# Performance work log

Measured on AMD Instinct MI355X. Metric: run time of the kernel, lower is better.

## Reference

```python
import jax, jax.numpy as jnp
import numpy as np

B, S, E, H = 4, 2048, 1024, 16
HD = E // H


def setup_inputs() -> dict:
    key = jax.random.key(0)
    ks = jax.random.split(key, 7)
    scale = 1.0 / np.sqrt(E)
    return {
        "query": jax.random.normal(ks[0], (B, S, E), dtype=jnp.float32),
        "key": jax.random.normal(ks[1], (B, S, E), dtype=jnp.float32),
        "value": jax.random.normal(ks[2], (B, S, E), dtype=jnp.float32),
        "Wqkv": jax.random.normal(ks[3], (3 * E, E), dtype=jnp.float32) * scale,
        "bqkv": jnp.zeros((3 * E,), dtype=jnp.float32),
        "Wout": jax.random.normal(ks[4], (E, E), dtype=jnp.float32) * scale,
        "bout": jnp.zeros((E,), dtype=jnp.float32),
    }


def reference(query, key, value, Wqkv, bqkv, Wout, bout):
    # key/value are ignored by the original module (QKV all from query).
    b, s, e = query.shape
    qkv = query @ Wqkv.T + bqkv                       # [B,S,3E]
    qkv = qkv.reshape(b, s, 3, H, HD)
    q = jnp.transpose(qkv[:, :, 0], (0, 2, 1, 3))     # [B,H,S,HD]
    k = jnp.transpose(qkv[:, :, 1], (0, 2, 1, 3))
    v = jnp.transpose(qkv[:, :, 2], (0, 2, 1, 3))
    # NOTE: original scales by embed_dim**0.5, not head_dim**0.5
    scores = jnp.einsum("bhqd,bhkd->bhqk", q, k) / jnp.sqrt(jnp.float32(e))
    attn = jax.nn.softmax(scores, axis=-1)            # dropout = identity (eval)
    out = jnp.einsum("bhqk,bhkd->bhqd", attn, v)      # [B,H,S,HD]
    out = jnp.transpose(out, (0, 2, 1, 3)).reshape(b, s, e)
    return out @ Wout.T + bout
```

## Files before the change

kernel.cpp:

```cpp
#include <hip/hip_runtime.h>
#include <stdint.h>


typedef __bf16 bf16;
typedef __bf16 bf16x8 __attribute__((ext_vector_type(8)));
typedef __bf16 bf16x4 __attribute__((ext_vector_type(4)));
typedef float  f32x4  __attribute__((ext_vector_type(4)));
typedef float  f32x16 __attribute__((ext_vector_type(16)));
typedef unsigned u32x2 __attribute__((ext_vector_type(2)));
typedef unsigned u32x4 __attribute__((ext_vector_type(4)));

#define MFMA16(a, b, c) __builtin_amdgcn_mfma_f32_16x16x32_bf16((a), (b), (c), 0, 0, 0)
#define MFMA32(a, b, c) __builtin_amdgcn_mfma_f32_32x32x16_bf16((a), (b), (c), 0, 0, 0)

__device__ __forceinline__ void gload16(const void* g, void* l) {
  __builtin_amdgcn_global_load_lds(
      (const __attribute__((address_space(1))) void*)g,
      (__attribute__((address_space(3))) void*)l, 16, 0, 0);
}

__device__ __forceinline__ uint32_t lds_off(const void* p) {
  return (uint32_t)(uintptr_t)(__attribute__((address_space(3))) const void*)p;
}

template <int IMM>
__device__ __forceinline__ bf16x4 tr16o(uint32_t off) {
  bf16x4 d;
  asm volatile("ds_read_b64_tr_b16 %0, %1 offset:%2" : "=&v"(d) : "v"(off), "i"(IMM));
  return d;
}

__device__ __forceinline__ bf16x8 vpack(bf16x4 lo, bf16x4 hi) {
  const u32x2 a = __builtin_bit_cast(u32x2, lo);
  const u32x2 b = __builtin_bit_cast(u32x2, hi);
  u32x4 t;
  t[0] = a[0]; t[1] = a[1]; t[2] = b[0]; t[3] = b[1];
  return __builtin_bit_cast(bf16x8, t);
}

__global__ __launch_bounds__(256) void cvt_all(const float* __restrict__ a,
                                               const float* __restrict__ b,
                                               const float* __restrict__ c,
                                               bf16* __restrict__ out,
                                               int na4, int nb4, int nc4) {
  const int i = blockIdx.x * 256 + threadIdx.x;
  const float4* src;
  int j = i;
  if (i < na4) {
    src = (const float4*)a;
  } else if (i < na4 + nb4) {
    src = (const float4*)b; j = i - na4;
  } else if (i < na4 + nb4 + nc4) {
    src = (const float4*)c; j = i - na4 - nb4;
  } else {
    return;
  }
  const float4 v = src[j];
  bf16x4 o;
  o[0] = (bf16)v.x; o[1] = (bf16)v.y; o[2] = (bf16)v.z; o[3] = (bf16)v.w;
  ((bf16x4*)out)[i] = o;
}

template <typename OutT>
__global__ __launch_bounds__(256, 2) void gemm_bt(const bf16* __restrict__ A,
                                                  const bf16* __restrict__ Bt,
                                                  const float* __restrict__ bias,
                                                  OutT* __restrict__ C,
                                                  int M, int N, int K,
                                                  int sc_lo, int sc_hi, float scv) {
  __shared__ bf16 As[2][128 * 32];
  __shared__ bf16 Bs[2][128 * 32];
  const int tid = threadIdx.x;
  const int lane = tid & 63, wid = tid >> 6;
  const int l15 = lane & 15, lg = lane >> 4;
  const int wr = wid >> 1, wc = wid & 1;
  const int row0 = blockIdx.y * 128, col0 = blockIdx.x * 128;
  const float cscale = (col0 >= sc_lo && col0 < sc_hi) ? scv : 1.0f;

  const char* asrc[2]; const char* bsrc[2];
  int ado[2];
#pragma unroll
  for (int j = 0; j < 2; ++j) {
    const int c = j * 256 + tid;
    const int r = c >> 2, cb = (c & 3) << 4;
    asrc[j] = (const char*)(A + (size_t)(row0 + r) * K) + cb;
    bsrc[j] = (const char*)(Bt + (size_t)(col0 + r) * K) + cb;
    ado[j] = c * 16;
  }

  f32x4 acc[4][4];
#pragma unroll
  for (int m = 0; m < 4; ++m)
#pragma unroll
    for (int n = 0; n < 4; ++n) acc[m][n] = (f32x4){0.f, 0.f, 0.f, 0.f};

  const int nIt = K >> 5;

  gload16(asrc[0], (char*)&As[0][0] + ado[0]);
  gload16(asrc[1], (char*)&As[0][0] + ado[1]);
  gload16(bsrc[0], (char*)&Bs[0][0] + ado[0]);
  gload16(bsrc[1], (char*)&Bs[0][0] + ado[1]);

  for (int it = 0; it < nIt; ++it) {
    const int cur = it & 1;
    if (it < nIt - 1) {
      const size_t off = (size_t)(it + 1) * 64;
      gload16(asrc[0] + off, (char*)&As[cur ^ 1][0] + ado[0]);
      gload16(asrc[1] + off, (char*)&As[cur ^ 1][0] + ado[1]);
      gload16(bsrc[0] + off, (char*)&Bs[cur ^ 1][0] + ado[0]);
      gload16(bsrc[1] + off, (char*)&Bs[cur ^ 1][0] + ado[1]);
      __builtin_amdgcn_sched_barrier(0);
      asm volatile("s_waitcnt vmcnt(4)" ::: "memory");
    } else {
      __builtin_amdgcn_sched_barrier(0);
      asm volatile("s_waitcnt vmcnt(0)" ::: "memory");
    }
    __builtin_amdgcn_s_barrier();
    __builtin_amdgcn_sched_barrier(0);

    const bf16* as = &As[cur][0];
    const bf16* bs = &Bs[cur][0];
    bf16x8 af[4], bfr[4];
#pragma unroll
    for (int m = 0; m < 4; ++m)
      af[m] = *(const bf16x8*)(as + ((wr * 64 + m * 16 + l15) << 5) + lg * 8);
#pragma unroll
    for (int n = 0; n < 4; ++n)
      bfr[n] = *(const bf16x8*)(bs + ((wc * 64 + n * 16 + l15) << 5) + lg * 8);
    __builtin_amdgcn_s_setprio(1);
#pragma unroll
    for (int m = 0; m < 4; ++m)
#pragma unroll
      for (int n = 0; n < 4; ++n) acc[m][n] = MFMA16(af[m], bfr[n], acc[m][n]);
    __builtin_amdgcn_s_setprio(0);
    __builtin_amdgcn_sched_barrier(0);
    __builtin_amdgcn_s_barrier();
  }

#pragma unroll
  for (int m = 0; m < 4; ++m) {
    const int grow0 = row0 + wr * 64 + m * 16 + lg * 4;
#pragma unroll
    for (int n = 0; n < 4; ++n) {
      const int gcol = col0 + wc * 64 + n * 16 + l15;
      const float bv = bias[gcol];
#pragma unroll
      for (int i = 0; i < 4; ++i)
        C[(size_t)(grow0 + i) * N + gcol] = (OutT)((acc[m][n][i] + bv) * cscale);
    }
  }
}

__global__ __launch_bounds__(512, 2) void attn_fwd(const bf16* __restrict__ qkv,
                                                   bf16* __restrict__ aout) {
  __shared__ bf16 Ks[2][128 * 64];
  __shared__ bf16 Vs[2][128 * 64];
  __shared__ float bc[8][32];

  const int bid = blockIdx.x;
  const int xcd = bid & 7, slot = bid >> 3;
  const int g = xcd + 8 * (slot >> 3);
  const int qblk = slot & 7;
  const int h = g & 15, b = g >> 4;

  const int tid = threadIdx.x, wid = tid >> 6, lane = tid & 63;
  const int l31 = lane & 31, hh = lane >> 5, l15 = lane & 15;
  const int b4 = (lane >> 4) & 1;
  const bf16* qbase = qkv + (size_t)b * 2048 * 3072;

  bf16x8 qf[4];
  {
    const bf16* qp = qbase + (size_t)(qblk * 256 + wid * 32 + l31) * 3072 + h * 64 + hh * 8;
    qf[0] = *(const bf16x8*)(qp);
    qf[1] = *(const bf16x8*)(qp + 16);
    qf[2] = *(const bf16x8*)(qp + 32);
    qf[3] = *(const bf16x8*)(qp + 48);
  }

  const char* ksrc[2]; const char* vsrc[2];
  int kdo[2], vdo[2];
#pragma unroll
  for (int j = 0; j < 2; ++j) {
    const int c = j * 512 + tid;
    {
      const int key = c >> 3;
      const int db = (((c & 7) ^ (key & 7)) << 4);
      ksrc[j] = (const char*)(qbase + (size_t)key * 3072 + 1024 + h * 64) + db;
      kdo[j] = c * 16;
    }
    {
      const int s = c >> 3, jj = c & 7;
      const int vkey = ((s >> 2) << 2) + (jj >> 1);
      const int vd = ((s & 3) << 4) + ((jj & 1) << 3);
      vsrc[j] = (const char*)(qbase + (size_t)vkey * 3072 + 2048 + h * 64 + vd);
      vdo[j] = c * 16;
    }
  }
  const size_t tadv = (size_t)128 * 3072 * 2;

  f32x16 o0, o1;
#pragma unroll
  for (int i = 0; i < 16; ++i) { o0[i] = 0.f; o1[i] = 0.f; }
  float lrow = 0.f;

  const uint32_t vbase = lds_off(&Vs[0][0]) + (uint32_t)(l15 * 8 + hh * 1024 + b4 * 128);

  gload16(ksrc[0], (char*)&Ks[0][0] + kdo[0]);
  gload16(ksrc[1], (char*)&Ks[0][0] + kdo[1]);
  gload16(vsrc[0], (char*)&Vs[0][0] + vdo[0]);
  gload16(vsrc[1], (char*)&Vs[0][0] + vdo[1]);

  for (int kt = 0; kt < 16; ++kt) {
    const int cur = kt & 1;
    if (kt < 15) {
      const size_t off = (size_t)(kt + 1) * tadv;
      char* kb = (char*)&Ks[cur ^ 1][0];
      char* vb = (char*)&Vs[cur ^ 1][0];
      gload16(ksrc[0] + off, kb + kdo[0]);
      gload16(ksrc[1] + off, kb + kdo[1]);
      gload16(vsrc[0] + off, vb + vdo[0]);
      gload16(vsrc[1] + off, vb + vdo[1]);
      __builtin_amdgcn_sched_barrier(0);
      asm volatile("s_waitcnt vmcnt(4)" ::: "memory");
    } else {
      __builtin_amdgcn_sched_barrier(0);
      asm volatile("s_waitcnt vmcnt(0)" ::: "memory");
    }
    __builtin_amdgcn_s_barrier();
    __builtin_amdgcn_sched_barrier(0);

#pragma unroll
    for (int half = 0; half < 2; ++half) {
      const char* ksb = (const char*)&Ks[cur][0] + half * 8192;
      const uint32_t vb_cur = vbase + (uint32_t)(cur * 16384 + half * 8192);

      f32x16 st0, st1;
#pragma unroll
      for (int i = 0; i < 16; ++i) { st0[i] = 0.f; st1[i] = 0.f; }
      __builtin_amdgcn_s_setprio(1);
#pragma unroll
      for (int k2 = 0; k2 < 4; ++k2) {
        const int dby = k2 * 32 + hh * 16;
        bf16x8 kf0 = *(const bf16x8*)(ksb + ((l31 * 128 + dby) ^ ((l31 & 7) << 4)));
        st0 = MFMA32(kf0, qf[k2], st0);
        bf16x8 kf1 = *(const bf16x8*)(ksb + (((l31 + 32) * 128 + dby) ^ ((l31 & 7) << 4)));
        st1 = MFMA32(kf1, qf[k2], st1);
      }
      __builtin_amdgcn_s_setprio(0);

      float ps0 = 0.f, ps1 = 0.f;
#pragma unroll
      for (int i = 0; i < 16; ++i) {
        st0[i] = __builtin_amdgcn_exp2f(st0[i]);
        st1[i] = __builtin_amdgcn_exp2f(st1[i]);
        ps0 += st0[i];
        ps1 += st1[i];
      }
      float ps = ps0 + ps1;
      ps += __shfl_xor(ps, 32);
      lrow += ps;

      uint32_t w[16];
#pragma unroll
      for (int j = 0; j < 8; ++j) {
        asm("v_cvt_pk_bf16_f32 %0, %1, %2" : "=v"(w[j]) : "v"(st0[2 * j]), "v"(st0[2 * j + 1]));
        asm("v_cvt_pk_bf16_f32 %0, %1, %2" : "=v"(w[8 + j]) : "v"(st1[2 * j]), "v"(st1[2 * j + 1]));
      }
#pragma unroll
      for (int g2 = 0; g2 < 4; ++g2) {
        asm volatile("v_permlane32_swap_b32 %0, %1" : "+v"(w[4 * g2]), "+v"(w[4 * g2 + 2]));
        asm volatile("v_permlane32_swap_b32 %0, %1" : "+v"(w[4 * g2 + 1]), "+v"(w[4 * g2 + 3]));
      }
      bf16x8 pf[4];
#pragma unroll
      for (int k2 = 0; k2 < 4; ++k2) {
        u32x4 t;
        t[0] = w[4 * k2]; t[1] = w[4 * k2 + 1]; t[2] = w[4 * k2 + 2]; t[3] = w[4 * k2 + 3];
        pf[k2] = __builtin_bit_cast(bf16x8, t);
      }

      {
        bf16x4 va[4], vb2[4];
        va[0] = tr16o<0 * 2048 + 0>(vb_cur);
        vb2[0] = tr16o<0 * 2048 + 512>(vb_cur);
        va[1] = tr16o<1 * 2048 + 0>(vb_cur);
        vb2[1] = tr16o<1 * 2048 + 512>(vb_cur);
        va[2] = tr16o<2 * 2048 + 0>(vb_cur);
        vb2[2] = tr16o<2 * 2048 + 512>(vb_cur);
        va[3] = tr16o<3 * 2048 + 0>(vb_cur);
        vb2[3] = tr16o<3 * 2048 + 512>(vb_cur);
        asm volatile("s_waitcnt lgkmcnt(0)" ::: "memory");
        __builtin_amdgcn_sched_barrier(0);
        __builtin_amdgcn_s_setprio(1);
#pragma unroll
        for (int k2 = 0; k2 < 4; ++k2)
          o0 = MFMA32(pf[k2], vpack(va[k2], vb2[k2]), o0);
        __builtin_amdgcn_s_setprio(0);
        va[0] = tr16o<0 * 2048 + 256 + 0>(vb_cur);
        vb2[0] = tr16o<0 * 2048 + 256 + 512>(vb_cur);
        va[1] = tr16o<1 * 2048 + 256 + 0>(vb_cur);
        vb2[1] = tr16o<1 * 2048 + 256 + 512>(vb_cur);
        va[2] = tr16o<2 * 2048 + 256 + 0>(vb_cur);
        vb2[2] = tr16o<2 * 2048 + 256 + 512>(vb_cur);
        va[3] = tr16o<3 * 2048 + 256 + 0>(vb_cur);
        vb2[3] = tr16o<3 * 2048 + 256 + 512>(vb_cur);
        asm volatile("s_waitcnt lgkmcnt(0)" ::: "memory");
        __builtin_amdgcn_sched_barrier(0);
        __builtin_amdgcn_s_setprio(1);
#pragma unroll
        for (int k2 = 0; k2 < 4; ++k2)
          o1 = MFMA32(pf[k2], vpack(va[k2], vb2[k2]), o1);
        __builtin_amdgcn_s_setprio(0);
      }
    }
    __builtin_amdgcn_sched_barrier(0);
    __builtin_amdgcn_s_barrier();
  }

  if (lane < 32) bc[wid][l31] = 1.0f / lrow;
  bf16* ob = aout + ((size_t)b * 2048 + qblk * 256 + wid * 32) * 1024 + h * 64;
#pragma unroll
  for (int r = 0; r < 16; ++r) {
    const int row = (r & 3) + 8 * (r >> 2) + 4 * hh;
    const float inv = bc[wid][row];
    ob[(size_t)row * 1024 + l31]      = (bf16)(o0[r] * inv);
    ob[(size_t)row * 1024 + 32 + l31] = (bf16)(o1[r] * inv);
  }
}

extern "C" void kernel_launch(void* const* d_in, const int* in_sizes, int n_in,
                              void* d_out, int out_size, void* d_ws, size_t ws_size,
                              hipStream_t stream) {
  const float* query = (const float*)d_in[0];
  const float* Wqkv = (const float*)d_in[3];
  const float* bqkv = (const float*)d_in[4];
  const float* Wout = (const float*)d_in[5];
  const float* bout = (const float*)d_in[6];
  float* out = (float*)d_out;

  constexpr int M = 8192;
  constexpr int E = 1024, E3 = 3072;
  constexpr float SC = 0.045084220f;

  bf16* q_bf    = (bf16*)d_ws;
  bf16* wqkv_bf = q_bf + (size_t)M * E;
  bf16* wout_bf = wqkv_bf + (size_t)E3 * E;
  bf16* qkv_bf  = wout_bf + (size_t)E * E;
  bf16* aout_bf = qkv_bf + (size_t)M * E3;

  constexpr int na4 = M * E / 4, nb4 = E3 * E / 4, nc4 = E * E / 4;
  cvt_all<<<(na4 + nb4 + nc4 + 255) / 256, 256, 0, stream>>>(
      query, Wqkv, Wout, q_bf, na4, nb4, nc4);

  gemm_bt<bf16><<<dim3(E3 / 128, M / 128), 256, 0, stream>>>(
      q_bf, wqkv_bf, bqkv, qkv_bf, M, E3, E, E, 2 * E, SC);
  attn_fwd<<<512, 512, 0, stream>>>(qkv_bf, aout_bf);
  gemm_bt<float><<<dim3(E / 128, M / 128), 256, 0, stream>>>(
      aout_bf, wout_bf, bout, out, M, E, E, 0, 0, 1.0f);
}
```

Before: 189.5 us.

## Rework GEMM to BK=64 tiles, XOR-swizzled LDS, and 32x32x16 MFMA

The projection GEMM now stages 128x64 K-slices per iteration instead of 128x32, which halves the number of loop iterations and barriers. Rows are XOR-swizzled by 16-byte chunk in LDS so the 128-byte-strided fragment reads avoid bank conflicts. The 16x16x32 MFMAs are replaced by 32x32x16 MFMAs on a 2x2 fragment grid, which means fewer instructions and fewer LDS reads per FLOP. LDS use doubles to 64 KB per block, which may limit occupancy at two blocks per CU, and the epilogue store pattern changes.

```diff
diff --git a/kernel.cpp b/kernel.cpp
--- a/kernel.cpp
+++ b/kernel.cpp
@@ -10,7 +10,6 @@
 typedef unsigned u32x2 __attribute__((ext_vector_type(2)));
 typedef unsigned u32x4 __attribute__((ext_vector_type(4)));
 
-#define MFMA16(a, b, c) __builtin_amdgcn_mfma_f32_16x16x32_bf16((a), (b), (c), 0, 0, 0)
 #define MFMA32(a, b, c) __builtin_amdgcn_mfma_f32_32x32x16_bf16((a), (b), (c), 0, 0, 0)
 
 __device__ __forceinline__ void gload16(const void* g, void* l) {
@@ -68,49 +67,55 @@
                                                   OutT* __restrict__ C,
                                                   int M, int N, int K,
                                                   int sc_lo, int sc_hi, float scv) {
-  __shared__ bf16 As[2][128 * 32];
-  __shared__ bf16 Bs[2][128 * 32];
+  __shared__ bf16 As[2][128 * 64];
+  __shared__ bf16 Bs[2][128 * 64];
   const int tid = threadIdx.x;
   const int lane = tid & 63, wid = tid >> 6;
-  const int l15 = lane & 15, lg = lane >> 4;
+  const int l31 = lane & 31, hh = lane >> 5;
   const int wr = wid >> 1, wc = wid & 1;
   const int row0 = blockIdx.y * 128, col0 = blockIdx.x * 128;
   const float cscale = (col0 >= sc_lo && col0 < sc_hi) ? scv : 1.0f;
 
-  const char* asrc[2]; const char* bsrc[2];
-  int ado[2];
-#pragma unroll
-  for (int j = 0; j < 2; ++j) {
-    const int c = j * 256 + tid;
-    const int r = c >> 2, cb = (c & 3) << 4;
-    asrc[j] = (const char*)(A + (size_t)(row0 + r) * K) + cb;
-    bsrc[j] = (const char*)(Bt + (size_t)(col0 + r) * K) + cb;
-    ado[j] = c * 16;
-  }
-
-  f32x4 acc[4][4];
-#pragma unroll
-  for (int m = 0; m < 4; ++m)
-#pragma unroll
-    for (int n = 0; n < 4; ++n) acc[m][n] = (f32x4){0.f, 0.f, 0.f, 0.f};
-
-  const int nIt = K >> 5;
-
-  gload16(asrc[0], (char*)&As[0][0] + ado[0]);
-  gload16(asrc[1], (char*)&As[0][0] + ado[1]);
-  gload16(bsrc[0], (char*)&Bs[0][0] + ado[0]);
-  gload16(bsrc[1], (char*)&Bs[0][0] + ado[1]);
+  const int srow = tid >> 3;
+  const int sso = ((tid & 7) ^ (srow & 7)) << 4;
+  const char* a0 = (const char*)(A + (size_t)(row0 + srow) * K) + sso;
+  const char* b0 = (const char*)(Bt + (size_t)(col0 + srow) * K) + sso;
+  const size_t rstride = (size_t)32 * K * 2;
+  const int d0 = tid * 16;
+
+  f32x16 acc[2][2];
+#pragma unroll
+  for (int mf = 0; mf < 2; ++mf)
+#pragma unroll
+    for (int nf = 0; nf < 2; ++nf)
+#pragma unroll
+      for (int r = 0; r < 16; ++r) acc[mf][nf][r] = 0.f;
+
+  const int nIt = K >> 6;
+
+  {
+    char* ad = (char*)&As[0][0] + d0;
+    char* bd = (char*)&Bs[0][0] + d0;
+#pragma unroll
+    for (int j = 0; j < 4; ++j) {
+      gload16(a0 + j * rstride, ad + j * 4096);
+      gload16(b0 + j * rstride, bd + j * 4096);
+    }
+  }
 
   for (int it = 0; it < nIt; ++it) {
     const int cur = it & 1;
     if (it < nIt - 1) {
-      const size_t off = (size_t)(it + 1) * 64;
-      gload16(asrc[0] + off, (char*)&As[cur ^ 1][0] + ado[0]);
-      gload16(asrc[1] + off, (char*)&As[cur ^ 1][0] + ado[1]);
-      gload16(bsrc[0] + off, (char*)&Bs[cur ^ 1][0] + ado[0]);
-      gload16(bsrc[1] + off, (char*)&Bs[cur ^ 1][0] + ado[1]);
+      const size_t ko = (size_t)(it + 1) * 128;
+      char* ad = (char*)&As[cur ^ 1][0] + d0;
+      char* bd = (char*)&Bs[cur ^ 1][0] + d0;
+#pragma unroll
+      for (int j = 0; j < 4; ++j) {
+        gload16(a0 + j * rstride + ko, ad + j * 4096);
+        gload16(b0 + j * rstride + ko, bd + j * 4096);
+      }
       __builtin_amdgcn_sched_barrier(0);
-      asm volatile("s_waitcnt vmcnt(4)" ::: "memory");
+      asm volatile("s_waitcnt vmcnt(8)" ::: "memory");
     } else {
       __builtin_amdgcn_sched_barrier(0);
       asm volatile("s_waitcnt vmcnt(0)" ::: "memory");
@@ -118,37 +123,39 @@
     __builtin_amdgcn_s_barrier();
     __builtin_amdgcn_sched_barrier(0);
 
-    const bf16* as = &As[cur][0];
-    const bf16* bs = &Bs[cur][0];
-    bf16x8 af[4], bfr[4];
-#pragma unroll
-    for (int m = 0; m < 4; ++m)
-      af[m] = *(const bf16x8*)(as + ((wr * 64 + m * 16 + l15) << 5) + lg * 8);
-#pragma unroll
-    for (int n = 0; n < 4; ++n)
-      bfr[n] = *(const bf16x8*)(bs + ((wc * 64 + n * 16 + l15) << 5) + lg * 8);
-    __builtin_amdgcn_s_setprio(1);
-#pragma unroll
-    for (int m = 0; m < 4; ++m)
-#pragma unroll
-      for (int n = 0; n < 4; ++n) acc[m][n] = MFMA16(af[m], bfr[n], acc[m][n]);
-    __builtin_amdgcn_s_setprio(0);
+    const char* as = (const char*)&As[cur][0];
+    const char* bs = (const char*)&Bs[cur][0];
+    const int rsw = (l31 & 7) << 4;
+#pragma unroll
+    for (int k2 = 0; k2 < 4; ++k2) {
+      const int kb = k2 * 32 + hh * 16;
+      bf16x8 af0 = *(const bf16x8*)(as + (((wr * 64 + l31) * 128 + kb) ^ rsw));
+      bf16x8 af1 = *(const bf16x8*)(as + (((wr * 64 + 32 + l31) * 128 + kb) ^ rsw));
+      bf16x8 bq0 = *(const bf16x8*)(bs + (((wc * 64 + l31) * 128 + kb) ^ rsw));
+      bf16x8 bq1 = *(const bf16x8*)(bs + (((wc * 64 + 32 + l31) * 128 + kb) ^ rsw));
+      __builtin_amdgcn_s_setprio(1);
+      acc[0][0] = MFMA32(af0, bq0, acc[0][0]);
+      acc[0][1] = MFMA32(af0, bq1, acc[0][1]);
+      acc[1][0] = MFMA32(af1, bq0, acc[1][0]);
+      acc[1][1] = MFMA32(af1, bq1, acc[1][1]);
+      __builtin_amdgcn_s_setprio(0);
+    }
     __builtin_amdgcn_sched_barrier(0);
     __builtin_amdgcn_s_barrier();
   }
 
 #pragma unroll
-  for (int m = 0; m < 4; ++m) {
-    const int grow0 = row0 + wr * 64 + m * 16 + lg * 4;
-#pragma unroll
-    for (int n = 0; n < 4; ++n) {
-      const int gcol = col0 + wc * 64 + n * 16 + l15;
+  for (int mf = 0; mf < 2; ++mf)
+#pragma unroll
+    for (int nf = 0; nf < 2; ++nf) {
+      const int gcol = col0 + wc * 64 + nf * 32 + l31;
       const float bv = bias[gcol];
 #pragma unroll
-      for (int i = 0; i < 4; ++i)
-        C[(size_t)(grow0 + i) * N + gcol] = (OutT)((acc[m][n][i] + bv) * cscale);
-    }
-  }
+      for (int r = 0; r < 16; ++r) {
+        const int grow = row0 + wr * 64 + mf * 32 + (r & 3) + 8 * (r >> 2) + 4 * hh;
+        C[(size_t)grow * N + gcol] = (OutT)((acc[mf][nf][r] + bv) * cscale);
+      }
+    }
 }
 
 __global__ __launch_bounds__(512, 2) void attn_fwd(const bf16* __restrict__ qkv,
```

Result: no change. 187.9 us, median of 2 (-0.8%).
